# Kernel optimization log

Measured on AMD Instinct MI355X. Metric: run time of the kernel, lower is better.

## Reference

```python
import jax, jax.numpy as jnp
import numpy as np

HOP = 256
FRAMELEN = 512
FILTERLEN = 64
WD = FILTERLEN // 2          # weights_delay default
WMIN, WMAX = -65535.0, 65535.0
MU = 0.05                    # LMS step size (concrete iterate)
B = 2
NFRAMES = 4096
T = FRAMELEN + HOP * (NFRAMES - 1)


def _unfold(a, size, step):
    # torch.Tensor.unfold along last dim -> (..., n_frames, size)
    n = (a.shape[-1] - size) // step + 1
    idx = np.arange(n)[:, None] * step + np.arange(size)[None, :]
    return a[..., idx]


def setup_inputs() -> dict:
    key = jax.random.key(0)
    kd, kx = jax.random.split(key)
    d = jax.random.normal(kd, (B, T), dtype=jnp.float32)
    x = jax.random.normal(kx, (T,), dtype=jnp.float32)
    return {"d": d, "x": x}


def reference(d, x):
    d_f = _unfold(d, FRAMELEN, HOP)            # (B, F, framelen)
    x_f = _unfold(x, FRAMELEN, HOP)[None]      # (1, F, framelen)
    Bn, F, _ = d_f.shape
    S = (FRAMELEN - FILTERLEN) - WD            # sequential steps per frame
    w0 = jnp.zeros((Bn, F, FILTERLEN), d.dtype)

    def step(w, t):
        # x window [t : t+filterlen]  (i = WD + t in the torch loop)
        xi = jax.lax.dynamic_slice_in_dim(x_f, t, FILTERLEN, axis=2)  # (1,F,K)
        d_est = jnp.sum(w * xi, axis=-1)       # einsum('ijk,pjk->ij', w, xi)
        e = d_f[..., WD + t] - d_est
        w = jnp.clip(w + MU * e[..., None] * xi, WMIN, WMAX)
        return w, (d_est, e)

    _, (d_est_s, e_s) = jax.lax.scan(step, w0, jnp.arange(S))

    def assemble(y):
        # (S,B,F) -> (B,F, framelen-filterlen), first WD slots stay zero
        y = jnp.moveaxis(y, 0, -1)
        return jnp.pad(y, ((0, 0), (0, 0), (WD, 0)))

    d_est = assemble(d_est_s)
    e = assemble(e_s)
    tail = FRAMELEN - HOP

    def ola(y):
        # first frame in full, then non-overlapping tail of each later frame
        return jnp.concatenate(
            [y[:, 0, :], y[:, 1:, tail:].reshape(y.shape[0], -1)], axis=-1)

    return ola(d_est), ola(e)
```

## Files before the change

kernel.cpp:

```cpp
#include <hip/hip_runtime.h>

#define HOP     256
#define WD      32
#define NFRM    4096
#define TLEN    1048832
#define LROW    786688
#define FPB     8
#define XSTR    484
#define DSTR    420
#define XQn     121
#define DQn     105
#define XTOT    (FPB*XSTR + 16)
#define DTOT    (2*FPB*DSTR + 8)

__device__ __forceinline__ float red16(float v) {
    v += __int_as_float(__builtin_amdgcn_update_dpp(0, __float_as_int(v), 0xB1,  0xF, 0xF, true));
    v += __int_as_float(__builtin_amdgcn_update_dpp(0, __float_as_int(v), 0x4E,  0xF, 0xF, true));
    v += __int_as_float(__builtin_amdgcn_update_dpp(0, __float_as_int(v), 0x141, 0xF, 0xF, true));
    v += __int_as_float(__builtin_amdgcn_update_dpp(0, __float_as_int(v), 0x140, 0xF, 0xF, true));
    return v;
}

#define CL(v) __builtin_amdgcn_fmed3f((v), -65535.0f, 65535.0f)

#define STEP1(X0,X1,X2,X3, DV, GV, J) do {                        \
    float p = w0 * (X0);                                          \
    p = fmaf(w1, (X1), p);                                        \
    p = fmaf(w2, (X2), p);                                        \
    p = fmaf(w3, (X3), p);                                        \
    float s  = red16(p);                                          \
    float gm = fmaf(-0.05f, s, (GV));                             \
    float e  = (DV) - s;                                          \
    so = (col == (J)) ? s : so;                                   \
    eo = (col == (J)) ? e : eo;                                   \
    w0 = CL(fmaf(gm, (X0), w0));                                  \
    w1 = CL(fmaf(gm, (X1), w1));                                  \
    w2 = CL(fmaf(gm, (X2), w2));                                  \
    w3 = CL(fmaf(gm, (X3), w3));                                  \
} while (0)

#define GROUP4(QA, QB, DQ4, GQ4, G) do {                          \
    float so = 0.f, eo = 0.f;                                     \
    STEP1(QA.x,QA.y,QA.z,QA.w, DQ4.x, GQ4.x, 0);                  \
    STEP1(QA.y,QA.z,QA.w,QB.x, DQ4.y, GQ4.y, 1);                  \
    STEP1(QA.z,QA.w,QB.x,QB.y, DQ4.z, GQ4.z, 2);                  \
    STEP1(QA.w,QB.x,QB.y,QB.z, DQ4.w, GQ4.w, 3);                  \
    if (((G) >= 56 || early) && col < 4) {                        \
        od[4*(G)+col] = so; oe[4*(G)+col] = eo; }                 \
} while (0)

__global__ void __launch_bounds__(256, 2)
lms_kernel(const float* __restrict__ dmat, const float* __restrict__ xvec,
           float* __restrict__ out)
{
    __shared__ __align__(16) float lx[XTOT];
    __shared__ __align__(16) float ld[DTOT];
    __shared__ __align__(16) float lg[DTOT];

    const int tid = threadIdx.x;
    const int f0  = blockIdx.x * FPB;

    for (int i = tid; i < 968 + 1680; i += 256) {
        if (i < 968) {
            int fr = i / XQn, k = i - fr * XQn;
            ((float4*)lx)[i] =
                *(const float4*)(xvec + (size_t)(f0 + fr) * HOP + 4 * k);
        } else {
            int j = i - 968;
            int idx = j / DQn, k = j - idx * DQn;
            int b = idx >> 3, r = idx & 7;
            float4 v = *(const float4*)(dmat + (size_t)b * TLEN
                                        + (size_t)(f0 + r) * HOP + WD + 4 * k);
            ((float4*)ld)[j] = v;
            float4 g;
            g.x = 0.05f * v.x; g.y = 0.05f * v.y;
            g.z = 0.05f * v.z; g.w = 0.05f * v.w;
            ((float4*)lg)[j] = g;
        }
    }
    __syncthreads();

    const int lane = tid & 63;
    const int wv   = tid >> 6;
    const int row  = lane >> 4;
    const int col  = lane & 15;
    const int fl   = 2 * wv + (row >> 1);
    const int b    = row & 1;
    const int f    = f0 + fl;
    const bool early = (f == 0);
    const int ci   = b * FPB + fl;

    const float4* __restrict__ xq = (const float4*)(lx + fl * XSTR + 4 * col);
    const float4* __restrict__ dq = (const float4*)(ld + ci * DSTR);
    const float4* __restrict__ gq = (const float4*)(lg + ci * DSTR);

    float* od = out + (size_t)b * LROW + 32 + (size_t)192 * f;
    float* oe = od + 2 * (size_t)LROW;

    if (blockIdx.x == 0 && tid < 128) {
        out[(size_t)(tid >> 5) * LROW + (tid & 31)] = 0.0f;
    }

    float w0 = 0.f, w1 = 0.f, w2 = 0.f, w3 = 0.f;

    float4 X0 = xq[0], X1 = xq[1], X2 = xq[2];
    float4 D0 = dq[0], G0 = gq[0];
    float4 D1 = dq[1], G1 = gq[1];

    for (int j = 0; j < 26; ++j) {
        const int g = 4 * j;
        float4 X3 = xq[g+3];  float4 D2 = dq[g+2];  float4 G2 = gq[g+2];
        GROUP4(X0, X1, D0, G0, g);

        X0 = xq[g+4];  float4 D3 = dq[g+3];  float4 G3 = gq[g+3];
        GROUP4(X1, X2, D1, G1, g+1);

        X1 = xq[g+5];  D0 = dq[g+4];  G0 = gq[g+4];
        GROUP4(X2, X3, D2, G2, g+2);

        X2 = xq[g+6];  D1 = dq[g+5];  G1 = gq[g+5];
        GROUP4(X3, X0, D3, G3, g+3);
    }
}

extern "C" void kernel_launch(void* const* d_in, const int* in_sizes, int n_in,
                              void* d_out, int out_size, void* d_ws, size_t ws_size,
                              hipStream_t stream) {
    const float* dmat = (const float*)d_in[0];
    const float* xvec = (const float*)d_in[1];
    float* out = (float*)d_out;

    hipLaunchKernelGGL(lms_kernel, dim3(NFRM / FPB), dim3(256), 0, stream,
                       dmat, xvec, out);
}
```

Before: 38.04 us.

## Shrink blocks to one wave, drop d buffer, batch outputs per 16 steps

Each block now holds one 64-lane wave covering 2 frames instead of 8, and more blocks are launched. The shared d copy is dropped: the error is rebuilt at store time as 20*(0.05*d - 0.05*s). Per-step outputs are gathered into one register with fma against precomputed one-hot column masks. Stores now happen once per 16 steps as full 16-lane writes instead of every 4 steps on 4 lanes. This cuts shared memory, register pressure from the D vectors, and store instructions, but the 20x rescale can add small rounding error and the smaller blocks raise launch overhead.

```diff
diff --git a/kernel.cpp b/kernel.cpp
--- a/kernel.cpp
+++ b/kernel.cpp
@@ -5,13 +5,12 @@
 #define NFRM    4096
 #define TLEN    1048832
 #define LROW    786688
-#define FPB     8
 #define XSTR    484
 #define DSTR    420
 #define XQn     121
 #define DQn     105
-#define XTOT    (FPB*XSTR + 16)
-#define DTOT    (2*FPB*DSTR + 8)
+#define XTOT    (2*XSTR + 16)
+#define GTOT    (4*DSTR + 8)
 
 __device__ __forceinline__ float red16(float v) {
     v += __int_as_float(__builtin_amdgcn_update_dpp(0, __float_as_int(v), 0xB1,  0xF, 0xF, true));
@@ -23,103 +22,115 @@
 
 #define CL(v) __builtin_amdgcn_fmed3f((v), -65535.0f, 65535.0f)
 
-#define STEP1(X0,X1,X2,X3, DV, GV, J) do {                        \
-    float p = w0 * (X0);                                          \
-    p = fmaf(w1, (X1), p);                                        \
-    p = fmaf(w2, (X2), p);                                        \
-    p = fmaf(w3, (X3), p);                                        \
+#define STEP1(Xa,Xb,Xc,Xd, GV, IND) do {                          \
+    float p = w0 * (Xa);                                          \
+    p = fmaf(w1, (Xb), p);                                        \
+    p = fmaf(w2, (Xc), p);                                        \
+    p = fmaf(w3, (Xd), p);                                        \
     float s  = red16(p);                                          \
+    so = fmaf((IND), s, so);                                      \
     float gm = fmaf(-0.05f, s, (GV));                             \
-    float e  = (DV) - s;                                          \
-    so = (col == (J)) ? s : so;                                   \
-    eo = (col == (J)) ? e : eo;                                   \
-    w0 = CL(fmaf(gm, (X0), w0));                                  \
-    w1 = CL(fmaf(gm, (X1), w1));                                  \
-    w2 = CL(fmaf(gm, (X2), w2));                                  \
-    w3 = CL(fmaf(gm, (X3), w3));                                  \
+    w0 = CL(fmaf(gm, (Xa), w0));                                  \
+    w1 = CL(fmaf(gm, (Xb), w1));                                  \
+    w2 = CL(fmaf(gm, (Xc), w2));                                  \
+    w3 = CL(fmaf(gm, (Xd), w3));                                  \
 } while (0)
 
-#define GROUP4(QA, QB, DQ4, GQ4, G) do {                          \
-    float so = 0.f, eo = 0.f;                                     \
-    STEP1(QA.x,QA.y,QA.z,QA.w, DQ4.x, GQ4.x, 0);                  \
-    STEP1(QA.y,QA.z,QA.w,QB.x, DQ4.y, GQ4.y, 1);                  \
-    STEP1(QA.z,QA.w,QB.x,QB.y, DQ4.z, GQ4.z, 2);                  \
-    STEP1(QA.w,QB.x,QB.y,QB.z, DQ4.w, GQ4.w, 3);                  \
-    if (((G) >= 56 || early) && col < 4) {                        \
-        od[4*(G)+col] = so; oe[4*(G)+col] = eo; }                 \
+#define GROUP4(QA, QB, GQ, Ia, Ib, Ic, Id) do {                   \
+    STEP1(QA.x,QA.y,QA.z,QA.w, GQ.x, Ia);                         \
+    STEP1(QA.y,QA.z,QA.w,QB.x, GQ.y, Ib);                         \
+    STEP1(QA.z,QA.w,QB.x,QB.y, GQ.z, Ic);                         \
+    STEP1(QA.w,QB.x,QB.y,QB.z, GQ.w, Id);                         \
 } while (0)
 
-__global__ void __launch_bounds__(256, 2)
+__global__ void __launch_bounds__(64, 2)
 lms_kernel(const float* __restrict__ dmat, const float* __restrict__ xvec,
            float* __restrict__ out)
 {
     __shared__ __align__(16) float lx[XTOT];
-    __shared__ __align__(16) float ld[DTOT];
-    __shared__ __align__(16) float lg[DTOT];
+    __shared__ __align__(16) float lg[GTOT];
 
     const int tid = threadIdx.x;
-    const int f0  = blockIdx.x * FPB;
+    const int f0  = blockIdx.x * 2;
 
-    for (int i = tid; i < 968 + 1680; i += 256) {
-        if (i < 968) {
-            int fr = i / XQn, k = i - fr * XQn;
+    for (int i = tid; i < 242 + 420; i += 64) {
+        if (i < 242) {
+            int fr = (i >= XQn) ? 1 : 0;
+            int k  = i - fr * XQn;
             ((float4*)lx)[i] =
                 *(const float4*)(xvec + (size_t)(f0 + fr) * HOP + 4 * k);
         } else {
-            int j = i - 968;
+            int j   = i - 242;
             int idx = j / DQn, k = j - idx * DQn;
-            int b = idx >> 3, r = idx & 7;
+            int b = idx >> 1, r = idx & 1;
             float4 v = *(const float4*)(dmat + (size_t)b * TLEN
                                         + (size_t)(f0 + r) * HOP + WD + 4 * k);
-            ((float4*)ld)[j] = v;
-            float4 g;
-            g.x = 0.05f * v.x; g.y = 0.05f * v.y;
-            g.z = 0.05f * v.z; g.w = 0.05f * v.w;
-            ((float4*)lg)[j] = g;
+            float4 g2;
+            g2.x = 0.05f * v.x; g2.y = 0.05f * v.y;
+            g2.z = 0.05f * v.z; g2.w = 0.05f * v.w;
+            ((float4*)lg)[j] = g2;
         }
     }
     __syncthreads();
 
     const int lane = tid & 63;
-    const int wv   = tid >> 6;
     const int row  = lane >> 4;
     const int col  = lane & 15;
-    const int fl   = 2 * wv + (row >> 1);
+    const int fl   = row >> 1;
     const int b    = row & 1;
     const int f    = f0 + fl;
     const bool early = (f == 0);
-    const int ci   = b * FPB + fl;
+    const int ci   = b * 2 + fl;
 
-    const float4* __restrict__ xq = (const float4*)(lx + fl * XSTR + 4 * col);
-    const float4* __restrict__ dq = (const float4*)(ld + ci * DSTR);
-    const float4* __restrict__ gq = (const float4*)(lg + ci * DSTR);
+    const float4* __restrict__ xq  = (const float4*)(lx + fl * XSTR + 4 * col);
+    const float4* __restrict__ gq  = (const float4*)(lg + ci * DSTR);
+    const float*  __restrict__ lgs = lg + ci * DSTR;
 
     float* od = out + (size_t)b * LROW + 32 + (size_t)192 * f;
     float* oe = od + 2 * (size_t)LROW;
 
-    if (blockIdx.x == 0 && tid < 128) {
-        out[(size_t)(tid >> 5) * LROW + (tid & 31)] = 0.0f;
+    if (blockIdx.x == 0) {
+        int pos = tid & 31;
+        for (int r2 = tid >> 5; r2 < 4; r2 += 2)
+            out[(size_t)r2 * LROW + pos] = 0.0f;
     }
+
+    const float i0  = (col ==  0) ? 1.f : 0.f, i1  = (col ==  1) ? 1.f : 0.f;
+    const float i2  = (col ==  2) ? 1.f : 0.f, i3  = (col ==  3) ? 1.f : 0.f;
+    const float i4  = (col ==  4) ? 1.f : 0.f, i5  = (col ==  5) ? 1.f : 0.f;
+    const float i6  = (col ==  6) ? 1.f : 0.f, i7  = (col ==  7) ? 1.f : 0.f;
+    const float i8  = (col ==  8) ? 1.f : 0.f, i9  = (col ==  9) ? 1.f : 0.f;
+    const float i10 = (col == 10) ? 1.f : 0.f, i11 = (col == 11) ? 1.f : 0.f;
+    const float i12 = (col == 12) ? 1.f : 0.f, i13 = (col == 13) ? 1.f : 0.f;
+    const float i14 = (col == 14) ? 1.f : 0.f, i15 = (col == 15) ? 1.f : 0.f;
 
     float w0 = 0.f, w1 = 0.f, w2 = 0.f, w3 = 0.f;
 
     float4 X0 = xq[0], X1 = xq[1], X2 = xq[2];
-    float4 D0 = dq[0], G0 = gq[0];
-    float4 D1 = dq[1], G1 = gq[1];
+    float4 G0 = gq[0], G1 = gq[1];
 
     for (int j = 0; j < 26; ++j) {
         const int g = 4 * j;
-        float4 X3 = xq[g+3];  float4 D2 = dq[g+2];  float4 G2 = gq[g+2];
-        GROUP4(X0, X1, D0, G0, g);
+        float so  = 0.f;
+        float gvs = lgs[16 * j + col];
 
-        X0 = xq[g+4];  float4 D3 = dq[g+3];  float4 G3 = gq[g+3];
-        GROUP4(X1, X2, D1, G1, g+1);
+        float4 X3 = xq[g+3];  float4 G2 = gq[g+2];
+        GROUP4(X0, X1, G0, i0,  i1,  i2,  i3);
 
-        X1 = xq[g+5];  D0 = dq[g+4];  G0 = gq[g+4];
-        GROUP4(X2, X3, D2, G2, g+2);
+        X0 = xq[g+4];         float4 G3 = gq[g+3];
+        GROUP4(X1, X2, G1, i4,  i5,  i6,  i7);
 
-        X2 = xq[g+6];  D1 = dq[g+5];  G1 = gq[g+5];
-        GROUP4(X3, X0, D3, G3, g+3);
+        X1 = xq[g+5];         G0 = gq[g+4];
+        GROUP4(X2, X3, G2, i8,  i9,  i10, i11);
+
+        X2 = xq[g+6];         G1 = gq[g+5];
+        GROUP4(X3, X0, G3, i12, i13, i14, i15);
+
+        if (j >= 14 || early) {
+            float gms = fmaf(-0.05f, so, gvs);
+            od[16 * j + col] = so;
+            oe[16 * j + col] = 20.0f * gms;
+        }
     }
 }
 
@@ -130,6 +141,6 @@
     const float* xvec = (const float*)d_in[1];
     float* out = (float*)d_out;
 
-    hipLaunchKernelGGL(lms_kernel, dim3(NFRM / FPB), dim3(256), 0, stream,
+    hipLaunchKernelGGL(lms_kernel, dim3(NFRM / 2), dim3(64), 0, stream,
                        dmat, xvec, out);
 }
```

Result: faster. 36.93 us, median of 2 (-2.9%).
